# Kernel optimization log

Hardware: AMD Instinct MI355X
Metric: run time of the kernel (lower is better)

The kernel has to match this reference:

```python
import jax, jax.numpy as jnp
import numpy as np
from jax import lax

B, T, E, H, L, V = 64, 512, 512, 1024, 2, 32000  # batch, seq, d_emb, d_hid, n_layer, n_vocab


def setup_inputs() -> dict:
    key = jax.random.key(0)
    ks = jax.random.split(key, 8)
    s = 0.03  # small init keeps tanh recurrence well-conditioned
    return {
        "src": jax.random.randint(ks[0], (B, T), 0, V),
        "emb_table": jax.random.normal(ks[1], (V, E), jnp.float32) * s,
        "W1": jax.random.normal(ks[2], (H, E), jnp.float32) * s,
        "b1": jnp.zeros((H,), jnp.float32),
        "W2": jax.random.normal(ks[3], (H, H), jnp.float32) * s,
        "b2": jnp.zeros((H,), jnp.float32),
        # layer 0 input dim = H; layers >0 input dim = 2H (bidirectional concat)
        "W_ih0": jax.random.normal(ks[4], (2, H, H), jnp.float32) * s,
        "W_ihL": jax.random.normal(ks[5], (L - 1, 2, H, 2 * H), jnp.float32) * s,
        "W_hh": jax.random.normal(ks[6], (L, 2, H, H), jnp.float32) * s,
        "b_ih": jnp.zeros((L, 2, H), jnp.float32),
        "b_hh": jnp.zeros((L, 2, H), jnp.float32),
    }


def _rnn_dir(x, Wih, Whh, bih, bhh, reverse):
    # x: [B, T, Din]. Precompute input projection as one big GEMM, then scan.
    pre = jnp.einsum('bti,hi->tbh', x, Wih) + bih  # [T, B, H]

    def step(h, p):
        h = jnp.tanh(p + h @ Whh.T + bhh)
        return h, h

    h0 = jnp.zeros((x.shape[0], Whh.shape[0]), x.dtype)
    hT, hs = lax.scan(step, h0, pre, reverse=reverse)
    return hT, jnp.transpose(hs, (1, 0, 2))  # final state [B,H], outputs [B,T,H]


def reference(src, emb_table, W1, b1, W2, b2, W_ih0, W_ihL, W_hh, b_ih, b_hh):
    # Embedding with padding_idx=0 (row zeroed)
    table = emb_table.at[0].set(0.0)
    x = table[src]  # [B, T, E]
    # emb_to_hid MLP (dropout is identity in eval mode)
    x = jax.nn.relu(x @ W1.T + b1)
    x = jax.nn.relu(x @ W2.T + b2)  # [B, T, H]
    finals = []
    inp = x
    for l in range(L):
        Wih = W_ih0 if l == 0 else W_ihL[l - 1]
        hf, of = _rnn_dir(inp, Wih[0], W_hh[l, 0], b_ih[l, 0], b_hh[l, 0], False)
        hb, ob = _rnn_dir(inp, Wih[1], W_hh[l, 1], b_ih[l, 1], b_hh[l, 1], True)
        finals += [hf, hb]
        inp = jnp.concatenate([of, ob], axis=-1)  # [B, T, 2H]
    # torch h_n layout: [n_layer * num_directions, B, H], layer-major, dir-minor
    return jnp.stack(finals, axis=0)
```

## Files before the change

### kernel.cpp

```cpp
#include <hip/hip_runtime.h>


typedef _Float16 f16;
typedef _Float16 f16x8 __attribute__((ext_vector_type(8)));
typedef _Float16 f16x4 __attribute__((ext_vector_type(4)));
typedef float f32x4 __attribute__((ext_vector_type(4)));

static const size_t MB_ = 1024ull * 1024ull;
static const size_t OFF_X0    = 0;
static const size_t OFF_X1    = 64 * MB_;
static const size_t OFF_EMB   = OFF_X1;
static const size_t OFF_MLP1  = 96 * MB_;
static const size_t OFF_H     = 192 * MB_;
static const size_t OFF_FLAGS = 192 * MB_ + 512 * 1024;
static const size_t OFF_BIAS  = 192 * MB_ + 576 * 1024;
static const size_t OFF_W1C   = 193 * MB_;
static const size_t OFF_W2C   = 194 * MB_;
static const size_t WS_NEED   = 196 * MB_;
static const size_t P_X0    = 0;
static const size_t P_X1    = 0;
static const size_t P_PRE   = 128 * MB_;
static const size_t P_EMB   = 128 * MB_;
static const size_t P_MLP1  = 160 * MB_;
static const size_t P_H     = 256 * MB_;
static const size_t P_FLAGS = 256 * MB_ + 512 * 1024;
static const size_t P_BIAS  = 256 * MB_ + 576 * 1024;
static const size_t P_W1C   = 257 * MB_;
static const size_t P_W2C   = 258 * MB_;
static const size_t P_WIH0C = 260 * MB_;
static const size_t P_WIHLC = 264 * MB_;
static const size_t WS_NEED2 = 272 * MB_;

__device__ __forceinline__ void gld16(const void* g, void* l) {
#if __has_builtin(__builtin_amdgcn_global_load_lds)
  __builtin_amdgcn_global_load_lds((const __attribute__((address_space(1))) void*)g,
                                   (__attribute__((address_space(3))) void*)l, 16, 0, 0);
#else
  *(f16x8*)l = *(const f16x8*)g;
#endif
}

__device__ __forceinline__ float tanh_fast(float x) {
  float ax = __builtin_fabsf(x);
  float e = __builtin_amdgcn_exp2f(ax * 2.8853900817779268f);
  float r = 1.0f - 2.0f * __builtin_amdgcn_rcpf(e + 1.0f);
  return __builtin_copysignf(r, x);
}


__global__ void zero_k(unsigned int* __restrict__ p, int n) {
  int i = blockIdx.x * blockDim.x + threadIdx.x;
  if (i < n) p[i] = 0u;
}

__global__ void cvt_k(const float* __restrict__ in, f16* __restrict__ out, int n4) {
  int i = blockIdx.x * blockDim.x + threadIdx.x;
  int stride = gridDim.x * blockDim.x;
  for (; i < n4; i += stride) {
    float4 v = ((const float4*)in)[i];
    f16x4 o = {(f16)v.x, (f16)v.y, (f16)v.z, (f16)v.w};
    ((f16x4*)out)[i] = o;
  }
}

__global__ void bias_k(const float* __restrict__ a, const float* __restrict__ b, float* __restrict__ o) {
  int i = blockIdx.x * blockDim.x + threadIdx.x;
  if (i < 4096) o[i] = a[i] + b[i];
}

__global__ void embed_k(const int* __restrict__ src, const float* __restrict__ tab, f16* __restrict__ out) {
  int m = blockIdx.x;
  int tid = threadIdx.x;
  int tok = src[m];
  f16x4 o = {(f16)0.f, (f16)0.f, (f16)0.f, (f16)0.f};
  if (tok != 0) {
    float4 v = *(const float4*)(tab + (size_t)tok * 512 + tid * 4);
    o[0] = (f16)v.x; o[1] = (f16)v.y; o[2] = (f16)v.z; o[3] = (f16)v.w;
  }
  *(f16x4*)(out + (size_t)m * 512 + tid * 4) = o;
}

template <int EPI>
__global__ __launch_bounds__(256) void gemm_f16(
    const f16* __restrict__ A, int lda, const f16* __restrict__ Bw,
    f16* __restrict__ out, const float* __restrict__ bias, int M, int N, int K) {
  __shared__ alignas(16) f16 As[4096];
  __shared__ alignas(16) f16 Bs[4096];
  const int nt = N >> 7;
  const int bx = blockIdx.x;
  const int tm = bx / nt, tn = bx - tm * nt;
  const int tid = threadIdx.x;
  const int l = tid & 63, w = tid >> 6;
  const int wr = w >> 1, wc = w & 1;
  const int srow = (w << 4) + (l >> 2);
  const int scol = (l & 3) << 3;
  const f16* Ab = A + (size_t)(tm * 128 + srow) * lda + scol;
  const f16* Bb = Bw + (size_t)(tn * 128 + srow) * K + scol;
  f32x4 acc[4][4];
#pragma unroll
  for (int i = 0; i < 4; i++)
#pragma unroll
    for (int j = 0; j < 4; j++) acc[i][j] = (f32x4){0.f, 0.f, 0.f, 0.f};
  const int ar = l & 15, ak = (l >> 4) << 3;
  for (int k0 = 0; k0 < K; k0 += 32) {
    gld16(Ab + k0, &As[tid * 8]);
    gld16(Ab + (size_t)64 * lda + k0, &As[tid * 8 + 2048]);
    gld16(Bb + k0, &Bs[tid * 8]);
    gld16(Bb + (size_t)64 * K + k0, &Bs[tid * 8 + 2048]);
    __syncthreads();
    f16x8 av[4], bv[4];
#pragma unroll
    for (int i = 0; i < 4; i++) av[i] = *(const f16x8*)&As[(wr * 64 + i * 16 + ar) * 32 + ak];
#pragma unroll
    for (int j = 0; j < 4; j++) bv[j] = *(const f16x8*)&Bs[(wc * 64 + j * 16 + ar) * 32 + ak];
#pragma unroll
    for (int i = 0; i < 4; i++)
#pragma unroll
      for (int j = 0; j < 4; j++)
        acc[i][j] = __builtin_amdgcn_mfma_f32_16x16x32_f16(av[i], bv[j], acc[i][j], 0, 0, 0);
    __syncthreads();
  }
  const int r0 = (l >> 4) << 2, c0 = l & 15;
#pragma unroll
  for (int i = 0; i < 4; i++) {
#pragma unroll
    for (int j = 0; j < 4; j++) {
      const int col = tn * 128 + wc * 64 + j * 16 + c0;
      const float bc = (EPI & 1) ? bias[col] : 0.f;
#pragma unroll
      for (int r = 0; r < 4; r++) {
        const int row = tm * 128 + wr * 64 + i * 16 + r0 + r;
        float v = acc[i][j][r];
        if (EPI & 1) { v += bc; v = v > 0.f ? v : 0.f; }
        if (EPI & 2) {
          const int b_ = row >> 9, t = row & 511;
          out[((size_t)(t * 64 + b_) << 10) + col] = (f16)v;
        } else {
          out[(size_t)row * N + col] = (f16)v;
        }
      }
    }
  }
}

template <int LAYER>
__global__ __launch_bounds__(512, 1) void rnn_scan(
    const f16* __restrict__ X, const float* __restrict__ Wih, const float* __restrict__ Whh,
    const float* __restrict__ bsum, f16* __restrict__ hbuf, unsigned int* __restrict__ flags,
    f16* __restrict__ seqout, float* __restrict__ dout) {
  constexpr int KX = LAYER ? 2048 : 1024;
  constexpr int XSH = LAYER ? 11 : 10;
  constexpr int NKX = KX / 128;
  constexpr int NKH = 8;
  const int bid = blockIdx.x;
  const int dir = bid >> 7, bg = (bid >> 6) & 1, cg = bid & 63;
  const int tid = threadIdx.x, l = tid & 63, w = tid >> 6;
  const int mi = w & 1, kq = w >> 1;
  __shared__ alignas(16) f16 Wl[16 * 1024];
  __shared__ alignas(16) f16 Wi[16 * KX];
  __shared__ f32x4 part[2][4][64];
  __shared__ alignas(16) f16 p2[32][16];
  __shared__ unsigned int cnt;
  const int ld = LAYER * 2 + dir;
  if (tid == 0) cnt = 0u;
  for (int ch = tid; ch < 2048; ch += 512) {
    const int n = ch >> 7, k0 = (ch & 127) << 3;
    const float* wp = Whh + (((size_t)(ld * 1024 + cg * 16 + n)) << 10) + k0;
    float4 v0 = *(const float4*)wp, v1 = *(const float4*)(wp + 4);
    f16x8 hv = {(f16)v0.x, (f16)v0.y, (f16)v0.z, (f16)v0.w,
                (f16)v1.x, (f16)v1.y, (f16)v1.z, (f16)v1.w};
    *(f16x8*)&Wl[(n << 10) + (k0 ^ ((n & 7) << 3))] = hv;
  }
  for (int ch = tid; ch < (16 * KX / 8); ch += 512) {
    const int n = ch >> (XSH - 3), k0 = (ch & (KX / 8 - 1)) << 3;
    const float* wp = Wih + ((size_t)(dir * 1024 + cg * 16 + n)) * KX + k0;
    float4 v0 = *(const float4*)wp, v1 = *(const float4*)(wp + 4);
    f16x8 hv = {(f16)v0.x, (f16)v0.y, (f16)v0.z, (f16)v0.w,
                (f16)v1.x, (f16)v1.y, (f16)v1.z, (f16)v1.w};
    *(f16x8*)&Wi[(n << XSH) + (k0 ^ ((n & 7) << 3))] = hv;
  }
  const float bn = bsum[(ld << 10) + cg * 16 + (l & 15)];
  f16* hD = hbuf + ((size_t)dir << 17);
  unsigned int* fl = flags + ((dir * 2 + bg) << 10);
  const int arow = bg * 32 + mi * 16 + (l & 15);
  const int akh = (kq << 8) + ((l >> 4) << 3);
  const int akx = kq * (KX / 4) + ((l >> 4) << 3);
  const int wn = l & 15;
  const int wsw = (wn & 7) << 3;

  f16x8 xv[NKX];
  {
    const int t0 = dir ? 511 : 0;
    const f16* xr = X + (((size_t)(t0 * 64 + arow)) << XSH) + akx;
#pragma unroll
    for (int i = 0; i < NKX; i++)
      asm volatile("global_load_dwordx4 %0, %1, off offset:%2"
                   : "=&v"(xv[i]) : "v"(xr), "i"(64 * i));
  }
  __syncthreads();

  for (int s = 0; s < 512; ++s) {
    const int t = dir ? (511 - s) : s;
    f32x4 acc = {0.f, 0.f, 0.f, 0.f};
    if (s > 0) {
      if (w == 7) {
        const unsigned int tgt = (unsigned int)(LAYER * 512 + s);
        unsigned int* fp = fl + l * 16;
        for (;;) {
          unsigned int f = __hip_atomic_load(fp, __ATOMIC_RELAXED, __HIP_MEMORY_SCOPE_AGENT);
          if (__all((int)(f >= tgt))) break;
        }
      }
      __syncthreads();
      const f16* hrow = hD + (((size_t)(s & 1)) << 16) + (((size_t)arow) << 10) + akh;
      f16x8 hv[NKH];
#pragma unroll
      for (int i = 0; i < NKH; i++)
        asm volatile("global_load_dwordx4 %0, %1, off offset:%2 sc0 sc1"
                     : "=&v"(hv[i]) : "v"(hrow), "i"(64 * i));
      asm volatile("s_waitcnt vmcnt(%0)" :: "i"(NKH) : "memory");
      __builtin_amdgcn_sched_barrier(0);
#pragma unroll
      for (int it = 0; it < NKX; ++it) {
        const int ko = akx + it * 32;
        f16x8 bv = *(const f16x8*)&Wi[(wn << XSH) + (ko ^ wsw)];
        acc = __builtin_amdgcn_mfma_f32_16x16x32_f16(xv[it], bv, acc, 0, 0, 0);
      }
      asm volatile("s_waitcnt vmcnt(0)" ::: "memory");
      __builtin_amdgcn_sched_barrier(0);
#pragma unroll
      for (int it = 0; it < NKH; ++it) {
        const int ko = akh + it * 32;
        f16x8 bv = *(const f16x8*)&Wl[(wn << 10) + (ko ^ wsw)];
        acc = __builtin_amdgcn_mfma_f32_16x16x32_f16(hv[it], bv, acc, 0, 0, 0);
      }
    } else {
      asm volatile("s_waitcnt vmcnt(0)" ::: "memory");
      __builtin_amdgcn_sched_barrier(0);
#pragma unroll
      for (int it = 0; it < NKX; ++it) {
        const int ko = akx + it * 32;
        f16x8 bv = *(const f16x8*)&Wi[(wn << XSH) + (ko ^ wsw)];
        acc = __builtin_amdgcn_mfma_f32_16x16x32_f16(xv[it], bv, acc, 0, 0, 0);
      }
    }
    part[mi][kq][l] = acc;
    __syncthreads();
    if (w < 2) {
      f32x4 sum = part[w][0][l];
      sum += part[w][1][l];
      sum += part[w][2][l];
      sum += part[w][3][l];
#pragma unroll
      for (int r = 0; r < 4; ++r) {
        const int row = ((l >> 4) << 2) + r;
        float v = tanh_fast(sum[r] + bn);
        p2[(w << 4) + row][l & 15] = (f16)v;
        if (s == 511) {
          const int b_ = bg * 32 + (w << 4) + row;
          dout[(((size_t)(ld * 64 + b_)) << 10) + cg * 16 + (l & 15)] = v;
        }
      }
      asm volatile("s_waitcnt lgkmcnt(0)" ::: "memory");
      __builtin_amdgcn_sched_barrier(0);
      if (l < 32) {
        const int rr = (w << 4) + (l >> 1), hf = l & 1;
        f16x8 pv = *(const f16x8*)&p2[rr][hf * 8];
        const int b_ = bg * 32 + rr;
        f16* hp = hD + (((size_t)((s + 1) & 1)) << 16) + (((size_t)b_) << 10) + cg * 16 + hf * 8;
        asm volatile("global_store_dwordx4 %0, %1, off sc0 sc1" :: "v"(hp), "v"(pv) : "memory");
        if (LAYER == 0) {
          f16* sp = seqout + (((size_t)(t * 64 + b_)) << 11) + (dir << 10) + cg * 16 + hf * 8;
          asm volatile("global_store_dwordx4 %0, %1, off" :: "v"(sp), "v"(pv) : "memory");
        }
      }
      asm volatile("s_waitcnt vmcnt(0)" ::: "memory");
      __builtin_amdgcn_sched_barrier(0);
      if (l == 0) {
        unsigned int old = __hip_atomic_fetch_add(&cnt, 1u, __ATOMIC_RELAXED,
                                                  __HIP_MEMORY_SCOPE_WORKGROUP);
        if (old == (unsigned int)(2 * s + 1))
          __hip_atomic_store(&fl[cg * 16], (unsigned int)(LAYER * 512 + s + 1),
                             __ATOMIC_RELAXED, __HIP_MEMORY_SCOPE_AGENT);
      }
    }
    if (s + 1 < 512) {
      const int tn_ = dir ? (511 - (s + 1)) : (s + 1);
      const f16* xr = X + (((size_t)(tn_ * 64 + arow)) << XSH) + akx;
#pragma unroll
      for (int i = 0; i < NKX; i++)
        asm volatile("global_load_dwordx4 %0, %1, off offset:%2"
                     : "=&v"(xv[i]) : "v"(xr), "i"(64 * i));
    }
  }
}

template <int LAYER>
__global__ __launch_bounds__(512, 1) void rnn_scan_pre(
    const f16* __restrict__ PRE,
    const float* __restrict__ Whh,
    const float* __restrict__ bsum,
    f16* __restrict__ hbuf,
    unsigned int* __restrict__ flags,
    f16* __restrict__ seqout,
    float* __restrict__ dout) {
  constexpr int NKH = 8;
  const int bid = blockIdx.x;
  const int dir = bid >> 7, bg = (bid >> 6) & 1, cg = bid & 63;
  const int tid = threadIdx.x, l = tid & 63, w = tid >> 6;
  const int mi = w & 1, kq = w >> 1;
  __shared__ alignas(16) f16 Wl[16 * 1024];
  __shared__ f32x4 part[2][4][64];
  __shared__ alignas(16) f16 p2[32][16];
  __shared__ unsigned int cnt;
  const int ld = LAYER * 2 + dir;
  if (tid == 0) cnt = 0u;
  for (int ch = tid; ch < 2048; ch += 512) {
    const int n = ch >> 7, k0 = (ch & 127) << 3;
    const float* wp = Whh + (((size_t)(ld * 1024 + cg * 16 + n)) << 10) + k0;
    float4 v0 = *(const float4*)wp, v1 = *(const float4*)(wp + 4);
    f16x8 hv = {(f16)v0.x, (f16)v0.y, (f16)v0.z, (f16)v0.w,
                (f16)v1.x, (f16)v1.y, (f16)v1.z, (f16)v1.w};
    *(f16x8*)&Wl[(n << 10) + (k0 ^ ((n & 7) << 3))] = hv;
  }
  const float bn = bsum[(ld << 10) + cg * 16 + (l & 15)];
  const f16* preD = PRE + (((size_t)dir) << 25);
  f16* hD = hbuf + ((size_t)dir << 17);
  unsigned int* fl = flags + ((dir * 2 + bg) << 10);
  const int arow = bg * 32 + mi * 16 + (l & 15);
  const int akh = (kq << 8) + ((l >> 4) << 3);
  const int wn = l & 15;
  const int wsw = (wn & 7) << 3;
  const int prow = bg * 32 + (w << 4) + ((l >> 4) << 2);
  const int pcol = cg * 16 + (l & 15);

  float pv0 = 0.f, pv1 = 0.f, pv2 = 0.f, pv3 = 0.f;
  if (w < 2) {
    const int t0 = dir ? 511 : 0;
    const f16* pp = preD + (((size_t)(t0 * 64 + prow)) << 10) + pcol;
    pv0 = (float)pp[0]; pv1 = (float)pp[1 << 10];
    pv2 = (float)pp[2 << 10]; pv3 = (float)pp[3 << 10];
  }
  __syncthreads();

  for (int s = 0; s < 512; ++s) {
    const int t = dir ? (511 - s) : s;
    f32x4 acc = {0.f, 0.f, 0.f, 0.f};
    if (s > 0) {
      if (w == 7) {
        const unsigned int tgt = (unsigned int)(LAYER * 512 + s);
        unsigned int* fp = fl + l * 16;
        for (;;) {
          unsigned int f = __hip_atomic_load(fp, __ATOMIC_RELAXED, __HIP_MEMORY_SCOPE_AGENT);
          if (__all((int)(f >= tgt))) break;
        }
      }
      __syncthreads();
      const f16* hrow = hD + (((size_t)(s & 1)) << 16) + (((size_t)arow) << 10) + akh;
      f16x8 hv[NKH];
#pragma unroll
      for (int i = 0; i < NKH; i++)
        asm volatile("global_load_dwordx4 %0, %1, off offset:%2 sc0 sc1"
                     : "=&v"(hv[i]) : "v"(hrow), "i"(64 * i));
      asm volatile("s_waitcnt vmcnt(0)" ::: "memory");
      __builtin_amdgcn_sched_barrier(0);
#pragma unroll
      for (int it = 0; it < NKH; ++it) {
        const int ko = akh + it * 32;
        f16x8 bv = *(const f16x8*)&Wl[(wn << 10) + (ko ^ wsw)];
        acc = __builtin_amdgcn_mfma_f32_16x16x32_f16(hv[it], bv, acc, 0, 0, 0);
      }
    }
    part[mi][kq][l] = acc;
    __syncthreads();
    if (w < 2) {
      f32x4 sum = part[w][0][l];
      sum += part[w][1][l];
      sum += part[w][2][l];
      sum += part[w][3][l];
      float pva[4] = {pv0, pv1, pv2, pv3};
#pragma unroll
      for (int r = 0; r < 4; ++r) {
        const int row = ((l >> 4) << 2) + r;
        float v = tanh_fast(sum[r] + pva[r] + bn);
        p2[(w << 4) + row][l & 15] = (f16)v;
        if (s == 511) {
          const int b_ = bg * 32 + (w << 4) + row;
          dout[(((size_t)(ld * 64 + b_)) << 10) + cg * 16 + (l & 15)] = v;
        }
      }
      asm volatile("s_waitcnt lgkmcnt(0)" ::: "memory");
      __builtin_amdgcn_sched_barrier(0);
      if (l < 32) {
        const int rr = (w << 4) + (l >> 1), hf = l & 1;
        f16x8 pv = *(const f16x8*)&p2[rr][hf * 8];
        const int b_ = bg * 32 + rr;
        f16* hp = hD + (((size_t)((s + 1) & 1)) << 16) + (((size_t)b_) << 10) + cg * 16 + hf * 8;
        asm volatile("global_store_dwordx4 %0, %1, off sc0 sc1" :: "v"(hp), "v"(pv) : "memory");
        if (LAYER == 0) {
          f16* sp = seqout + (((size_t)(t * 64 + b_)) << 11) + (dir << 10) + cg * 16 + hf * 8;
          asm volatile("global_store_dwordx4 %0, %1, off" :: "v"(sp), "v"(pv) : "memory");
        }
      }
      asm volatile("s_waitcnt vmcnt(0)" ::: "memory");
      __builtin_amdgcn_sched_barrier(0);
      if (l == 0) {
        unsigned int old = __hip_atomic_fetch_add(&cnt, 1u, __ATOMIC_RELAXED,
                                                  __HIP_MEMORY_SCOPE_WORKGROUP);
        if (old == (unsigned int)(2 * s + 1))
          __hip_atomic_store(&fl[cg * 16], (unsigned int)(LAYER * 512 + s + 1),
                             __ATOMIC_RELAXED, __HIP_MEMORY_SCOPE_AGENT);
      }
      if (s + 1 < 512) {
        const int tn_ = dir ? (511 - (s + 1)) : (s + 1);
        const f16* pp = preD + (((size_t)(tn_ * 64 + prow)) << 10) + pcol;
        pv0 = (float)pp[0]; pv1 = (float)pp[1 << 10];
        pv2 = (float)pp[2 << 10]; pv3 = (float)pp[3 << 10];
      }
    }
  }
}


extern "C" void kernel_launch(void* const* d_in, const int* in_sizes, int n_in,
                              void* d_out, int out_size, void* d_ws, size_t ws_size,
                              hipStream_t stream) {
  const int* src    = (const int*)d_in[0];
  const float* emb  = (const float*)d_in[1];
  const float* W1   = (const float*)d_in[2];
  const float* b1   = (const float*)d_in[3];
  const float* W2   = (const float*)d_in[4];
  const float* b2   = (const float*)d_in[5];
  const float* Wih0 = (const float*)d_in[6];
  const float* WihL = (const float*)d_in[7];
  const float* Whh  = (const float*)d_in[8];
  const float* bih  = (const float*)d_in[9];
  const float* bhh  = (const float*)d_in[10];
  float* out = (float*)d_out;
  char* ws = (char*)d_ws;

  if (ws_size >= WS_NEED2) {
    f16* X0   = (f16*)(ws + P_X0);
    f16* X1   = (f16*)(ws + P_X1);
    f16* PRE  = (f16*)(ws + P_PRE);
    f16* EMB  = (f16*)(ws + P_EMB);
    f16* MLP1 = (f16*)(ws + P_MLP1);
    f16* HB   = (f16*)(ws + P_H);
    unsigned int* FLAGS = (unsigned int*)(ws + P_FLAGS);
    float* BIAS = (float*)(ws + P_BIAS);
    f16* W1C  = (f16*)(ws + P_W1C);
    f16* W2C  = (f16*)(ws + P_W2C);
    f16* WIH0C = (f16*)(ws + P_WIH0C);
    f16* WIHLC = (f16*)(ws + P_WIHLC);

    cvt_k<<<256, 256, 0, stream>>>(W1, W1C, 131072);
    cvt_k<<<256, 256, 0, stream>>>(W2, W2C, 262144);
    cvt_k<<<512, 256, 0, stream>>>(Wih0, WIH0C, 524288);
    cvt_k<<<512, 256, 0, stream>>>(WihL, WIHLC, 1048576);
    bias_k<<<16, 256, 0, stream>>>(bih, bhh, BIAS);
    zero_k<<<16, 256, 0, stream>>>(FLAGS, 4096);

    embed_k<<<32768, 128, 0, stream>>>(src, emb, EMB);
    gemm_f16<1><<<2048, 256, 0, stream>>>(EMB, 512, W1C, MLP1, b1, 32768, 1024, 512);
    gemm_f16<3><<<2048, 256, 0, stream>>>(MLP1, 1024, W2C, X0, b2, 32768, 1024, 1024);

    gemm_f16<0><<<2048, 256, 0, stream>>>(X0, 1024, WIH0C, PRE, nullptr, 32768, 1024, 1024);
    gemm_f16<0><<<2048, 256, 0, stream>>>(X0, 1024, WIH0C + (1u << 20), PRE + (1ull << 25),
                                          nullptr, 32768, 1024, 1024);
    rnn_scan_pre<0><<<256, 512, 0, stream>>>(PRE, Whh, BIAS, HB, FLAGS, X1, out);

    gemm_f16<0><<<2048, 256, 0, stream>>>(X1, 2048, WIHLC, PRE, nullptr, 32768, 1024, 2048);
    gemm_f16<0><<<2048, 256, 0, stream>>>(X1, 2048, WIHLC + (1u << 21), PRE + (1ull << 25),
                                          nullptr, 32768, 1024, 2048);
    rnn_scan_pre<1><<<256, 512, 0, stream>>>(PRE, Whh, BIAS, HB, FLAGS, nullptr, out);
    return;
  }

  if (ws_size < WS_NEED) {
    zero_k<<<(out_size + 255) / 256, 256, 0, stream>>>((unsigned int*)d_out, out_size);
    return;
  }

  f16* X0   = (f16*)(ws + OFF_X0);
  f16* X1   = (f16*)(ws + OFF_X1);
  f16* EMB  = (f16*)(ws + OFF_EMB);
  f16* MLP1 = (f16*)(ws + OFF_MLP1);
  f16* HB   = (f16*)(ws + OFF_H);
  unsigned int* FLAGS = (unsigned int*)(ws + OFF_FLAGS);
  float* BIAS = (float*)(ws + OFF_BIAS);
  f16* W1C  = (f16*)(ws + OFF_W1C);
  f16* W2C  = (f16*)(ws + OFF_W2C);

  cvt_k<<<256, 256, 0, stream>>>(W1, W1C, 131072);
  cvt_k<<<256, 256, 0, stream>>>(W2, W2C, 262144);
  bias_k<<<16, 256, 0, stream>>>(bih, bhh, BIAS);
  zero_k<<<16, 256, 0, stream>>>(FLAGS, 4096);

  embed_k<<<32768, 128, 0, stream>>>(src, emb, EMB);
  gemm_f16<1><<<2048, 256, 0, stream>>>(EMB, 512, W1C, MLP1, b1, 32768, 1024, 512);
  gemm_f16<3><<<2048, 256, 0, stream>>>(MLP1, 1024, W2C, X0, b2, 32768, 1024, 1024);

  rnn_scan<0><<<256, 512, 0, stream>>>(X0, Wih0, Whh, BIAS, HB, FLAGS, X1, out);
  rnn_scan<1><<<256, 512, 0, stream>>>(X1, WihL, Whh, BIAS, HB, FLAGS, nullptr, out);
}
```

Measured before the change: 5.898 ms.

## Use fused layer-0 scan with hoisted GEMM for layer 1 and remap blocks

Replaces the all-precomputed path with a hybrid. Layer 0 always uses the fused rnn_scan, which computes the input projection inside the recurrence. Layer 1 precomputes its input projection with a new GEMM that converts fp32 weights on the fly, then runs a scan-only kernel. That kernel loads the precomputed values asynchronously with raw ushort loads and waits on them late. The block-to-(dir, batch-group, column-group) mapping is also interleaved, which changes how cooperating workgroups are placed across CUs. The workspace layout is reorganised, and the separate weight-conversion launches for Wih are dropped.

```diff
diff --git a/kernel.cpp b/kernel.cpp
--- a/kernel.cpp
+++ b/kernel.cpp
@@ -17,19 +17,12 @@
 static const size_t OFF_W1C   = 193 * MB_;
 static const size_t OFF_W2C   = 194 * MB_;
 static const size_t WS_NEED   = 196 * MB_;
-static const size_t P_X0    = 0;
-static const size_t P_X1    = 0;
-static const size_t P_PRE   = 128 * MB_;
-static const size_t P_EMB   = 128 * MB_;
-static const size_t P_MLP1  = 160 * MB_;
-static const size_t P_H     = 256 * MB_;
-static const size_t P_FLAGS = 256 * MB_ + 512 * 1024;
-static const size_t P_BIAS  = 256 * MB_ + 576 * 1024;
-static const size_t P_W1C   = 257 * MB_;
-static const size_t P_W2C   = 258 * MB_;
-static const size_t P_WIH0C = 260 * MB_;
-static const size_t P_WIHLC = 264 * MB_;
-static const size_t WS_NEED2 = 272 * MB_;
+static const size_t P_PRE1D0 = 0;
+static const size_t P_PRE1D1 = 192 * MB_;
+static const size_t P_HB1    = 64 * MB_;
+static const size_t P_FL1    = 64 * MB_ + 512 * 1024;
+static const size_t P_BIAS1  = 64 * MB_ + 528 * 1024;
+static const size_t WS_NEED2 = 256 * MB_;
 
 __device__ __forceinline__ void gld16(const void* g, void* l) {
 #if __has_builtin(__builtin_amdgcn_global_load_lds)
@@ -143,6 +136,70 @@
   }
 }
 
+__global__ __launch_bounds__(256) void gemm_b32(
+    const f16* __restrict__ A, int lda, const float* __restrict__ Bw,
+    f16* __restrict__ out, int M, int N, int K) {
+  __shared__ alignas(16) f16 As[4096];
+  __shared__ alignas(16) f16 Bs[4096];
+  const int nt = N >> 7;
+  const int bx = blockIdx.x;
+  const int tm = bx / nt, tn = bx - tm * nt;
+  const int tid = threadIdx.x;
+  const int l = tid & 63, w = tid >> 6;
+  const int wr = w >> 1, wc = w & 1;
+  const int srow = (w << 4) + (l >> 2);
+  const int scol = (l & 3) << 3;
+  const f16* Ab = A + (size_t)(tm * 128 + srow) * lda + scol;
+  const int brow = tid >> 1, bcol = (tid & 1) << 4;
+  const float* Bb = Bw + (size_t)(tn * 128 + brow) * K + bcol;
+  f32x4 acc[4][4];
+#pragma unroll
+  for (int i = 0; i < 4; i++)
+#pragma unroll
+    for (int j = 0; j < 4; j++) acc[i][j] = (f32x4){0.f, 0.f, 0.f, 0.f};
+  const int ar = l & 15, ak = (l >> 4) << 3;
+  for (int k0 = 0; k0 < K; k0 += 32) {
+    gld16(Ab + k0, &As[tid * 8]);
+    gld16(Ab + (size_t)64 * lda + k0, &As[tid * 8 + 2048]);
+    {
+      const float* bp = Bb + k0;
+      float4 u0 = *(const float4*)(bp + 0), u1 = *(const float4*)(bp + 4);
+      float4 u2 = *(const float4*)(bp + 8), u3 = *(const float4*)(bp + 12);
+      f16x8 h0 = {(f16)u0.x, (f16)u0.y, (f16)u0.z, (f16)u0.w,
+                  (f16)u1.x, (f16)u1.y, (f16)u1.z, (f16)u1.w};
+      f16x8 h1 = {(f16)u2.x, (f16)u2.y, (f16)u2.z, (f16)u2.w,
+                  (f16)u3.x, (f16)u3.y, (f16)u3.z, (f16)u3.w};
+      *(f16x8*)&Bs[brow * 32 + bcol] = h0;
+      *(f16x8*)&Bs[brow * 32 + bcol + 8] = h1;
+    }
+    __syncthreads();
+    f16x8 av[4], bv[4];
+#pragma unroll
+    for (int i = 0; i < 4; i++) av[i] = *(const f16x8*)&As[(wr * 64 + i * 16 + ar) * 32 + ak];
+#pragma unroll
+    for (int j = 0; j < 4; j++) bv[j] = *(const f16x8*)&Bs[(wc * 64 + j * 16 + ar) * 32 + ak];
+#pragma unroll
+    for (int i = 0; i < 4; i++)
+#pragma unroll
+      for (int j = 0; j < 4; j++)
+        acc[i][j] = __builtin_amdgcn_mfma_f32_16x16x32_f16(av[i], bv[j], acc[i][j], 0, 0, 0);
+    __syncthreads();
+  }
+  const int r0 = (l >> 4) << 2, c0 = l & 15;
+#pragma unroll
+  for (int i = 0; i < 4; i++) {
+#pragma unroll
+    for (int j = 0; j < 4; j++) {
+      const int col = tn * 128 + wc * 64 + j * 16 + c0;
+#pragma unroll
+      for (int r = 0; r < 4; r++) {
+        const int row = tm * 128 + wr * 64 + i * 16 + r0 + r;
+        out[(size_t)row * N + col] = (f16)acc[i][j][r];
+      }
+    }
+  }
+}
+
 template <int LAYER>
 __global__ __launch_bounds__(512, 1) void rnn_scan(
     const f16* __restrict__ X, const float* __restrict__ Wih, const float* __restrict__ Whh,
@@ -153,7 +210,9 @@
   constexpr int NKX = KX / 128;
   constexpr int NKH = 8;
   const int bid = blockIdx.x;
-  const int dir = bid >> 7, bg = (bid >> 6) & 1, cg = bid & 63;
+  const int g_ = (bid & 7) >> 1;
+  const int dir = g_ >> 1, bg = g_ & 1;
+  const int cg = ((bid & 1) << 5) | (bid >> 3);
   const int tid = threadIdx.x, l = tid & 63, w = tid >> 6;
   const int mi = w & 1, kq = w >> 1;
   __shared__ alignas(16) f16 Wl[16 * 1024];
@@ -295,25 +354,26 @@
   }
 }
 
-template <int LAYER>
-__global__ __launch_bounds__(512, 1) void rnn_scan_pre(
-    const f16* __restrict__ PRE,
+__global__ __launch_bounds__(512, 1) void rnn_scan_pre1(
+    const f16* __restrict__ PRE0,
+    const f16* __restrict__ PRE1,
     const float* __restrict__ Whh,
     const float* __restrict__ bsum,
     f16* __restrict__ hbuf,
     unsigned int* __restrict__ flags,
-    f16* __restrict__ seqout,
     float* __restrict__ dout) {
   constexpr int NKH = 8;
   const int bid = blockIdx.x;
-  const int dir = bid >> 7, bg = (bid >> 6) & 1, cg = bid & 63;
+  const int g_ = (bid & 7) >> 1;
+  const int dir = g_ >> 1, bg = g_ & 1;
+  const int cg = ((bid & 1) << 5) | (bid >> 3);
   const int tid = threadIdx.x, l = tid & 63, w = tid >> 6;
   const int mi = w & 1, kq = w >> 1;
   __shared__ alignas(16) f16 Wl[16 * 1024];
   __shared__ f32x4 part[2][4][64];
   __shared__ alignas(16) f16 p2[32][16];
   __shared__ unsigned int cnt;
-  const int ld = LAYER * 2 + dir;
+  const int ld = 2 + dir;
   if (tid == 0) cnt = 0u;
   for (int ch = tid; ch < 2048; ch += 512) {
     const int n = ch >> 7, k0 = (ch & 127) << 3;
@@ -323,8 +383,9 @@
                 (f16)v1.x, (f16)v1.y, (f16)v1.z, (f16)v1.w};
     *(f16x8*)&Wl[(n << 10) + (k0 ^ ((n & 7) << 3))] = hv;
   }
-  const float bn = bsum[(ld << 10) + cg * 16 + (l & 15)];
-  const f16* preD = PRE + (((size_t)dir) << 25);
+  const int pcol = cg * 16 + (l & 15);
+  const float bn = bsum[(ld << 10) + pcol];
+  const f16* preD = dir ? PRE1 : PRE0;
   f16* hD = hbuf + ((size_t)dir << 17);
   unsigned int* fl = flags + ((dir * 2 + bg) << 10);
   const int arow = bg * 32 + mi * 16 + (l & 15);
@@ -332,23 +393,24 @@
   const int wn = l & 15;
   const int wsw = (wn & 7) << 3;
   const int prow = bg * 32 + (w << 4) + ((l >> 4) << 2);
-  const int pcol = cg * 16 + (l & 15);
-
-  float pv0 = 0.f, pv1 = 0.f, pv2 = 0.f, pv3 = 0.f;
+
+  unsigned int pu0 = 0, pu1 = 0, pu2 = 0, pu3 = 0;
   if (w < 2) {
     const int t0 = dir ? 511 : 0;
-    const f16* pp = preD + (((size_t)(t0 * 64 + prow)) << 10) + pcol;
-    pv0 = (float)pp[0]; pv1 = (float)pp[1 << 10];
-    pv2 = (float)pp[2 << 10]; pv3 = (float)pp[3 << 10];
+    const f16* ppA = preD + (((size_t)(t0 * 64 + prow)) << 10) + pcol;
+    const f16* ppB = ppA + 2048;
+    asm volatile("global_load_ushort %0, %1, off" : "=&v"(pu0) : "v"(ppA));
+    asm volatile("global_load_ushort %0, %1, off offset:2048" : "=&v"(pu1) : "v"(ppA));
+    asm volatile("global_load_ushort %0, %1, off" : "=&v"(pu2) : "v"(ppB));
+    asm volatile("global_load_ushort %0, %1, off offset:2048" : "=&v"(pu3) : "v"(ppB));
   }
   __syncthreads();
 
   for (int s = 0; s < 512; ++s) {
-    const int t = dir ? (511 - s) : s;
     f32x4 acc = {0.f, 0.f, 0.f, 0.f};
     if (s > 0) {
       if (w == 7) {
-        const unsigned int tgt = (unsigned int)(LAYER * 512 + s);
+        const unsigned int tgt = (unsigned int)s;
         unsigned int* fp = fl + l * 16;
         for (;;) {
           unsigned int f = __hip_atomic_load(fp, __ATOMIC_RELAXED, __HIP_MEMORY_SCOPE_AGENT);
@@ -374,11 +436,17 @@
     part[mi][kq][l] = acc;
     __syncthreads();
     if (w < 2) {
+      asm volatile("s_waitcnt vmcnt(0)" ::: "memory");
+      __builtin_amdgcn_sched_barrier(0);
+      float pva[4];
+      pva[0] = (float)__builtin_bit_cast(f16, (unsigned short)pu0);
+      pva[1] = (float)__builtin_bit_cast(f16, (unsigned short)pu1);
+      pva[2] = (float)__builtin_bit_cast(f16, (unsigned short)pu2);
+      pva[3] = (float)__builtin_bit_cast(f16, (unsigned short)pu3);
       f32x4 sum = part[w][0][l];
       sum += part[w][1][l];
       sum += part[w][2][l];
       sum += part[w][3][l];
-      float pva[4] = {pv0, pv1, pv2, pv3};
 #pragma unroll
       for (int r = 0; r < 4; ++r) {
         const int row = ((l >> 4) << 2) + r;
@@ -386,7 +454,7 @@
         p2[(w << 4) + row][l & 15] = (f16)v;
         if (s == 511) {
           const int b_ = bg * 32 + (w << 4) + row;
-          dout[(((size_t)(ld * 64 + b_)) << 10) + cg * 16 + (l & 15)] = v;
+          dout[(((size_t)(ld * 64 + b_)) << 10) + pcol] = v;
         }
       }
       asm volatile("s_waitcnt lgkmcnt(0)" ::: "memory");
@@ -397,10 +465,6 @@
         const int b_ = bg * 32 + rr;
         f16* hp = hD + (((size_t)((s + 1) & 1)) << 16) + (((size_t)b_) << 10) + cg * 16 + hf * 8;
         asm volatile("global_store_dwordx4 %0, %1, off sc0 sc1" :: "v"(hp), "v"(pv) : "memory");
-        if (LAYER == 0) {
-          f16* sp = seqout + (((size_t)(t * 64 + b_)) << 11) + (dir << 10) + cg * 16 + hf * 8;
-          asm volatile("global_store_dwordx4 %0, %1, off" :: "v"(sp), "v"(pv) : "memory");
-        }
       }
       asm volatile("s_waitcnt vmcnt(0)" ::: "memory");
       __builtin_amdgcn_sched_barrier(0);
@@ -408,14 +472,17 @@
         unsigned int old = __hip_atomic_fetch_add(&cnt, 1u, __ATOMIC_RELAXED,
                                                   __HIP_MEMORY_SCOPE_WORKGROUP);
         if (old == (unsigned int)(2 * s + 1))
-          __hip_atomic_store(&fl[cg * 16], (unsigned int)(LAYER * 512 + s + 1),
+          __hip_atomic_store(&fl[cg * 16], (unsigned int)(s + 1),
                              __ATOMIC_RELAXED, __HIP_MEMORY_SCOPE_AGENT);
       }
       if (s + 1 < 512) {
         const int tn_ = dir ? (511 - (s + 1)) : (s + 1);
-        const f16* pp = preD + (((size_t)(tn_ * 64 + prow)) << 10) + pcol;
-        pv0 = (float)pp[0]; pv1 = (float)pp[1 << 10];
-        pv2 = (float)pp[2 << 10]; pv3 = (float)pp[3 << 10];
+        const f16* ppA = preD + (((size_t)(tn_ * 64 + prow)) << 10) + pcol;
+        const f16* ppB = ppA + 2048;
+        asm volatile("global_load_ushort %0, %1, off" : "=&v"(pu0) : "v"(ppA));
+        asm volatile("global_load_ushort %0, %1, off offset:2048" : "=&v"(pu1) : "v"(ppA));
+        asm volatile("global_load_ushort %0, %1, off" : "=&v"(pu2) : "v"(ppB));
+        asm volatile("global_load_ushort %0, %1, off offset:2048" : "=&v"(pu3) : "v"(ppB));
       }
     }
   }
@@ -439,43 +506,6 @@
   float* out = (float*)d_out;
   char* ws = (char*)d_ws;
 
-  if (ws_size >= WS_NEED2) {
-    f16* X0   = (f16*)(ws + P_X0);
-    f16* X1   = (f16*)(ws + P_X1);
-    f16* PRE  = (f16*)(ws + P_PRE);
-    f16* EMB  = (f16*)(ws + P_EMB);
-    f16* MLP1 = (f16*)(ws + P_MLP1);
-    f16* HB   = (f16*)(ws + P_H);
-    unsigned int* FLAGS = (unsigned int*)(ws + P_FLAGS);
-    float* BIAS = (float*)(ws + P_BIAS);
-    f16* W1C  = (f16*)(ws + P_W1C);
-    f16* W2C  = (f16*)(ws + P_W2C);
-    f16* WIH0C = (f16*)(ws + P_WIH0C);
-    f16* WIHLC = (f16*)(ws + P_WIHLC);
-
-    cvt_k<<<256, 256, 0, stream>>>(W1, W1C, 131072);
-    cvt_k<<<256, 256, 0, stream>>>(W2, W2C, 262144);
-    cvt_k<<<512, 256, 0, stream>>>(Wih0, WIH0C, 524288);
-    cvt_k<<<512, 256, 0, stream>>>(WihL, WIHLC, 1048576);
-    bias_k<<<16, 256, 0, stream>>>(bih, bhh, BIAS);
-    zero_k<<<16, 256, 0, stream>>>(FLAGS, 4096);
-
-    embed_k<<<32768, 128, 0, stream>>>(src, emb, EMB);
-    gemm_f16<1><<<2048, 256, 0, stream>>>(EMB, 512, W1C, MLP1, b1, 32768, 1024, 512);
-    gemm_f16<3><<<2048, 256, 0, stream>>>(MLP1, 1024, W2C, X0, b2, 32768, 1024, 1024);
-
-    gemm_f16<0><<<2048, 256, 0, stream>>>(X0, 1024, WIH0C, PRE, nullptr, 32768, 1024, 1024);
-    gemm_f16<0><<<2048, 256, 0, stream>>>(X0, 1024, WIH0C + (1u << 20), PRE + (1ull << 25),
-                                          nullptr, 32768, 1024, 1024);
-    rnn_scan_pre<0><<<256, 512, 0, stream>>>(PRE, Whh, BIAS, HB, FLAGS, X1, out);
-
-    gemm_f16<0><<<2048, 256, 0, stream>>>(X1, 2048, WIHLC, PRE, nullptr, 32768, 1024, 2048);
-    gemm_f16<0><<<2048, 256, 0, stream>>>(X1, 2048, WIHLC + (1u << 21), PRE + (1ull << 25),
-                                          nullptr, 32768, 1024, 2048);
-    rnn_scan_pre<1><<<256, 512, 0, stream>>>(PRE, Whh, BIAS, HB, FLAGS, nullptr, out);
-    return;
-  }
-
   if (ws_size < WS_NEED) {
     zero_k<<<(out_size + 255) / 256, 256, 0, stream>>>((unsigned int*)d_out, out_size);
     return;
@@ -501,5 +531,23 @@
   gemm_f16<3><<<2048, 256, 0, stream>>>(MLP1, 1024, W2C, X0, b2, 32768, 1024, 1024);
 
   rnn_scan<0><<<256, 512, 0, stream>>>(X0, Wih0, Whh, BIAS, HB, FLAGS, X1, out);
+
+  if (ws_size >= WS_NEED2) {
+    f16* PRE1D0 = (f16*)(ws + P_PRE1D0);
+    f16* PRE1D1 = (f16*)(ws + P_PRE1D1);
+    f16* HB1    = (f16*)(ws + P_HB1);
+    unsigned int* FLAGS1 = (unsigned int*)(ws + P_FL1);
+    float* BIAS1 = (float*)(ws + P_BIAS1);
+
+    gemm_b32<<<2048, 256, 0, stream>>>(X1, 2048, WihL, PRE1D0, 32768, 1024, 2048);
+    gemm_b32<<<2048, 256, 0, stream>>>(X1, 2048, WihL + (1u << 21), PRE1D1, 32768, 1024, 2048);
+
+    zero_k<<<16, 256, 0, stream>>>(FLAGS1, 4096);
+    bias_k<<<16, 256, 0, stream>>>(bih, bhh, BIAS1);
+
+    rnn_scan_pre1<<<256, 512, 0, stream>>>(PRE1D0, PRE1D1, Whh, BIAS1, HB1, FLAGS1, out);
+    return;
+  }
+
   rnn_scan<1><<<256, 512, 0, stream>>>(X1, WihL, Whh, BIAS, HB, FLAGS, nullptr, out);
 }
```

New measurement: 5.126 ms. -13.1%, faster.
